# Optimization experiments

Measured on AMD Instinct MI355X. Metric: run time of the kernel, lower is better.

The kernel has to match this reference:

```python
import jax, jax.numpy as jnp
import numpy as np

TOPK = 5
LAMBDA_ALIGN_K = 16.0
MOM = 0.9          # EMA momentum
DEFAULT_SCORE = 0.5  # EMA bank default (bank starts empty)
EPS = 1e-8
NEG = 1.0e9


def pairwise_cosine(X):
    # torch F.normalize: X / max(||X||, eps)
    n = jnp.linalg.norm(X, axis=-1, keepdims=True)
    Xn = X / jnp.maximum(n, EPS)
    sim = Xn @ Xn.T
    return jnp.clip(sim, -1.0 + EPS, 1.0 - EPS)


def knn_mask(sim, allowed_base, topk=TOPK):
    B = sim.shape[0]
    eye = jnp.eye(B, dtype=sim.dtype)
    allowed = allowed_base * (1.0 - eye)
    masked = sim - NEG * eye
    masked = jnp.where(allowed < 0.5, -NEG, masked)
    masked = jnp.where(masked < 0.0, -NEG, masked)
    cand = (masked > 0).sum(axis=1)
    k = min(topk, max(B - 1, 1))
    keep_row = (cand >= topk).astype(sim.dtype)
    keep = keep_row[:, None] * keep_row[None, :]
    idx = jax.lax.top_k(masked, k)[1]                       # [B, k]
    M = jnp.zeros_like(sim).at[jnp.arange(B)[:, None], idx].set(1.0)
    M = jnp.maximum(M, M.T)
    return M * allowed * keep


def build_intra(sim, same, topk=TOPK):
    M = knn_mask(sim, same, topk)
    A = jnp.maximum(sim * M, 0.0) * same
    return A, M


def pga_loss(feats_sub, labels_sub):
    # feats_sub: [L, b, d]
    L = feats_sub.shape[0]
    same = (labels_sub[:, None] == labels_sub[None, :]).astype(jnp.float32)
    sims = jax.vmap(pairwise_cosine)(feats_sub)             # [L, b, b]
    A, M = jax.vmap(lambda s: build_intra(s, same))(sims)   # [L, b, b] each

    # EMA degree-based scores (no-grad in original; bank starts empty so
    # fetch-after-update == mom*default + (1-mom)*score_cur)
    S_intra = jnp.maximum(sims * same, 0.0)
    deg = jnp.maximum((S_intra > 0).sum(axis=2).astype(jnp.float32), 1.0)
    score_cur = jax.nn.sigmoid(S_intra.sum(axis=2) / deg)   # [L, b]
    ema = jax.lax.stop_gradient(MOM * DEFAULT_SCORE + (1.0 - MOM) * score_cur)

    # layer-pair masked MSE alignment, target detached
    A_deep = A[1:]
    A_tgt = jax.lax.stop_gradient(A[:-1])
    M_eff = jnp.maximum(M[:-1], M[1:])                      # [L-1, b, b]
    W = ema[:-1, :, None] * ema[:-1, None, :]               # [L-1, b, b]
    diff2 = (A_deep - A_tgt) ** 2 * W
    num = (diff2 * M_eff).sum(axis=(1, 2))
    den = jnp.maximum((M_eff * W).sum(axis=(1, 2)), EPS)
    terms = jnp.where(M_eff.sum(axis=(1, 2)) > 0, num / den, 0.0)
    raw = terms.sum() / max(L - 1, 1)
    return LAMBDA_ALIGN_K * raw


def setup_inputs() -> dict:
    key = jax.random.key(0)
    k1, k2 = jax.random.split(key)
    feats_final = jax.random.normal(k1, (8, 2048, 512), dtype=jnp.float32)
    labels = jax.random.randint(k2, (2048,), 0, 128).astype(jnp.int64)
    sample_ids = jnp.arange(2048, dtype=jnp.int64)
    return {"feats_final": feats_final, "labels": labels, "sample_ids": sample_ids}


def reference(feats_final, labels, sample_ids):
    # candidate subset from last layer (no-grad in original)
    X_last = feats_final[-1]
    S_last = pairwise_cosine(X_last)
    same_full = (labels[:, None] == labels[None, :]).astype(jnp.float32)
    _, M_last = build_intra(S_last, same_full)
    cand_mask = (M_last > 0).sum(axis=1) > 0
    idx_sub = jnp.nonzero(cand_mask)[0]  # eager (concrete) subselection
    feats_sub = feats_final[:, idx_sub]  # [L, b, d]
    labels_sub = labels[idx_sub]
    return pga_loss(feats_sub, labels_sub)
```

## Files before the change

### kernel.cpp

```cpp
#include <hip/hip_runtime.h>
#include <cmath>

#define NB   2048
#define ND   512
#define NL   8
#define NLAB 128
#define MAXM 64
#define TOPK_ 5
#define NTH  256
#define MAXSLOT 9
#define GSTRIDE (MAXM*MAXM)

#define SLOT_DECL(s) int off##s = -1; int lds##s = 0; float4 pre##s;
#define SLOT_INIT(s) { int idx = tid + (s)*NTH; if (idx < (m << 5)) { \
    int i = idx >> 5, k4 = idx & 31; \
    off##s = (g_s[i] << 9) + (k4 << 2); \
    lds##s = i * 132 + (k4 << 2); \
    pre##s = *(const float4*)(X + off##s); } }
#define SLOT_STORE(s) if (off##s >= 0) *(float4*)(XtF + lds##s) = pre##s;
#define SLOT_FETCH(s, kcn) if (off##s >= 0) pre##s = *(const float4*)(X + off##s + (kcn));

__global__ __launch_bounds__(NTH) void k_gram(
    const float* __restrict__ feats, const int* __restrict__ labels,
    float* __restrict__ G, int* __restrict__ cnt,
    unsigned long long* __restrict__ insub)
{
    __shared__ int wsum[4];
    __shared__ int g_s[MAXM];
    __shared__ float Xt[MAXM][132];
    __shared__ float rinvp[64];
    __shared__ unsigned long long tops_s[64];
    __shared__ unsigned char keep_s[64];
    float* XtF = &Xt[0][0];
    int c = blockIdx.x, l = blockIdx.y, tid = threadIdx.x;
    int lane = tid & 63, wv = tid >> 6;

    int my[8]; int n = 0; int base_i = tid * 8;
    for (int t = 0; t < 8; ++t) {
        int i = base_i + t;
        if (labels[i] == c) my[n++] = i;
    }
    int scan = n;
    #pragma unroll
    for (int off = 1; off < 64; off <<= 1) {
        int v = __shfl_up(scan, off);
        if (lane >= off) scan += v;
    }
    if (lane == 63) wsum[wv] = scan;
    __syncthreads();
    int w0 = wsum[0], w1 = wsum[1], w2 = wsum[2], w3 = wsum[3];
    int m = w0 + w1 + w2 + w3; if (m > MAXM) m = MAXM;
    int base = (wv > 0 ? w0 : 0) + (wv > 1 ? w1 : 0) + (wv > 2 ? w2 : 0);
    int excl = base + scan - n;
    for (int t = 0; t < n; ++t) {
        int slot = excl + t;
        if (slot < MAXM) g_s[slot] = my[t];
    }
    if (l == 0 && tid == 0) cnt[c] = m;
    __syncthreads();
    if (m == 0) {
        if (l == 7 && tid == 0) insub[c] = 0ull;
        return;
    }

    const float* X = feats + (size_t)l * NB * ND;

    SLOT_DECL(0) SLOT_DECL(1) SLOT_DECL(2) SLOT_DECL(3)
    SLOT_DECL(4) SLOT_DECL(5) SLOT_DECL(6) SLOT_DECL(7)
    SLOT_INIT(0) SLOT_INIT(1) SLOT_INIT(2) SLOT_INIT(3)
    SLOT_INIT(4) SLOT_INIT(5) SLOT_INIT(6) SLOT_INIT(7)

    const int P = m * (m + 1) / 2;
    float acc0[MAXSLOT], acc1[MAXSLOT];
    short is_[MAXSLOT], js_[MAXSLOT];
    int ns = 0;
    for (int p = tid; p < P; p += NTH) {
        int i = (int)((sqrtf(8.0f * (float)p + 1.0f) - 1.0f) * 0.5f);
        while (((i + 1) * (i + 2)) / 2 <= p) ++i;
        while ((i * (i + 1)) / 2 > p) --i;
        is_[ns] = (short)i;
        js_[ns] = (short)(p - (i * (i + 1)) / 2);
        acc0[ns] = 0.0f; acc1[ns] = 0.0f;
        ++ns;
    }

    for (int kc = 0; kc < ND; kc += 128) {
        if (kc) __syncthreads();
        SLOT_STORE(0) SLOT_STORE(1) SLOT_STORE(2) SLOT_STORE(3)
        SLOT_STORE(4) SLOT_STORE(5) SLOT_STORE(6) SLOT_STORE(7)
        __syncthreads();
        if (kc + 128 < ND) {
            int kcn = kc + 128;
            SLOT_FETCH(0, kcn) SLOT_FETCH(1, kcn) SLOT_FETCH(2, kcn) SLOT_FETCH(3, kcn)
            SLOT_FETCH(4, kcn) SLOT_FETCH(5, kcn) SLOT_FETCH(6, kcn) SLOT_FETCH(7, kcn)
        }
        for (int s = 0; s < ns; ++s) {
            int i = is_[s], j = js_[s];
            float a0 = acc0[s], a1 = acc1[s];
            #pragma unroll
            for (int k4 = 0; k4 < 32; ++k4) {
                float4 a = *(const float4*)&Xt[i][k4 << 2];
                float4 b = *(const float4*)&Xt[j][k4 << 2];
                a0 = fmaf(a.x, b.x, a0); a1 = fmaf(a.y, b.y, a1);
                a0 = fmaf(a.z, b.z, a0); a1 = fmaf(a.w, b.w, a1);
            }
            acc0[s] = a0; acc1[s] = a1;
        }
    }
    float* Gc = G + ((size_t)l * NLAB + c) * GSTRIDE;
    for (int s = 0; s < ns; ++s) {
        int i = is_[s], j = js_[s];
        float v = acc0[s] + acc1[s];
        Gc[i * MAXM + j] = v;
        Gc[j * MAXM + i] = v;
    }
    if (l != 7) return;

    float (*Gs)[65] = (float(*)[65])(&Xt[0][0]);
    __syncthreads();
    for (int s = 0; s < ns; ++s) {
        int i = is_[s], j = js_[s];
        float v = acc0[s] + acc1[s];
        Gs[i][j] = v; Gs[j][i] = v;
    }
    if (tid < m) for (int j = m; j < 64; ++j) Gs[tid][j] = -2.0f;
    __syncthreads();
    if (tid < 64) {
        rinvp[tid] = (tid < m) ? 1.0f / fmaxf(sqrtf(Gs[tid][tid]), 1e-8f) : 0.0f;
        keep_s[tid] = 0; tops_s[tid] = 0ull;
    }
    __syncthreads();
    unsigned long long tops = 0ull; bool keep = false;
    if (tid < m) {
        float ri = rinvp[tid];
        float v0=-1.f,v1=-1.f,v2=-1.f,v3=-1.f,v4=-1.f;
        int i0=0,i1=0,i2=0,i3=0,i4=0, cand=0;
        #pragma unroll 8
        for (int j = 0; j < 64; ++j) {
            float raw = Gs[tid][j];
            float v = fminf(fmaxf(raw * ri * rinvp[j], -1.0f), 1.0f);
            if (raw == -2.0f) v = -2.0f;
            if (v > 0.0f && j != tid) {
                ++cand;
                if      (v > v0) { v4=v3;i4=i3; v3=v2;i3=i2; v2=v1;i2=i1; v1=v0;i1=i0; v0=v;i0=j; }
                else if (v > v1) { v4=v3;i4=i3; v3=v2;i3=i2; v2=v1;i2=i1; v1=v;i1=j; }
                else if (v > v2) { v4=v3;i4=i3; v3=v2;i3=i2; v2=v;i2=j; }
                else if (v > v3) { v4=v3;i4=i3; v3=v;i3=j; }
                else if (v > v4) { v4=v;i4=j; }
            }
        }
        keep = (cand >= TOPK_);
        if (keep) tops = (1ull<<i0)|(1ull<<i1)|(1ull<<i2)|(1ull<<i3)|(1ull<<i4);
        keep_s[tid] = keep ? 1 : 0; tops_s[tid] = tops;
    }
    __syncthreads();
    unsigned long long Mrow = 0ull;
    if (tid < m && keep) {
        for (int j = 0; j < 64; ++j) {
            if (j == tid || !keep_s[j]) continue;
            if (((tops >> j) & 1ull) || ((tops_s[j] >> tid) & 1ull)) Mrow |= (1ull << j);
        }
    }
    if (tid < 64) {
        unsigned long long b = __ballot(Mrow != 0ull);
        if (tid == 0) insub[c] = b;
    }
}

__device__ __forceinline__ void load_tile(
    const float* __restrict__ Gc, int m, int tid, float (*Gs)[65], float* rinv)
{
    if (tid < 64) rinv[tid] = (tid < m) ? 1.0f / fmaxf(sqrtf(Gc[tid * MAXM + tid]), 1e-8f) : 0.0f;
    __syncthreads();
    int tot = m << 4;
    for (int idx4 = tid; idx4 < tot; idx4 += NTH) {
        int i = idx4 >> 4, j0 = (idx4 & 15) << 2;
        float4 raw = *(const float4*)(Gc + i * MAXM + j0);
        float ri = rinv[i];
        Gs[i][j0 + 0] = (j0 + 0 < m) ? fminf(fmaxf(raw.x * ri * rinv[j0 + 0], -1.0f), 1.0f) : -2.0f;
        Gs[i][j0 + 1] = (j0 + 1 < m) ? fminf(fmaxf(raw.y * ri * rinv[j0 + 1], -1.0f), 1.0f) : -2.0f;
        Gs[i][j0 + 2] = (j0 + 2 < m) ? fminf(fmaxf(raw.z * ri * rinv[j0 + 2], -1.0f), 1.0f) : -2.0f;
        Gs[i][j0 + 3] = (j0 + 3 < m) ? fminf(fmaxf(raw.w * ri * rinv[j0 + 3], -1.0f), 1.0f) : -2.0f;
    }
    __syncthreads();
}

__global__ __launch_bounds__(NTH) void k_decide(
    const float* __restrict__ G, const int* __restrict__ cnt,
    const unsigned long long* __restrict__ insub,
    unsigned long long* __restrict__ Mbits, float* __restrict__ ema)
{
    __shared__ float Gs[64][65];
    __shared__ float rinv[64];
    __shared__ unsigned long long tops_s[64];
    __shared__ unsigned char keep_s[64];
    int c = blockIdx.x, l = blockIdx.y, tid = threadIdx.x;
    int m = cnt[c]; if (m > MAXM) m = MAXM;
    if (m == 0) return;
    unsigned long long sub = insub[c];

    const float* Gc = G + ((size_t)l * NLAB + c) * GSTRIDE;
    load_tile(Gc, m, tid, Gs, rinv);
    if (tid < 64) { keep_s[tid] = 0; tops_s[tid] = 0ull; }
    __syncthreads();
    unsigned long long tops = 0ull; bool keep = false; bool act = false;
    float emaval = 0.0f;
    if (tid < m) {
        act = (sub >> tid) & 1ull;
        if (act) {
            float v0=-1.f,v1=-1.f,v2=-1.f,v3=-1.f,v4=-1.f;
            int i0=0,i1=0,i2=0,i3=0,i4=0, cand=0, dg=0;
            float rs = 0.0f;
            #pragma unroll 8
            for (int j = 0; j < 64; ++j) {
                float v = Gs[tid][j];
                if (!((sub >> j) & 1ull)) v = -2.0f;
                if (v > 0.0f) {
                    rs += v; ++dg;
                    if (j != tid) {
                        ++cand;
                        if      (v > v0) { v4=v3;i4=i3; v3=v2;i3=i2; v2=v1;i2=i1; v1=v0;i1=i0; v0=v;i0=j; }
                        else if (v > v1) { v4=v3;i4=i3; v3=v2;i3=i2; v2=v1;i2=i1; v1=v;i1=j; }
                        else if (v > v2) { v4=v3;i4=i3; v3=v2;i3=i2; v2=v;i2=j; }
                        else if (v > v3) { v4=v3;i4=i3; v3=v;i3=j; }
                        else if (v > v4) { v4=v;i4=j; }
                    }
                }
            }
            keep = (cand >= TOPK_);
            if (keep) tops = (1ull<<i0)|(1ull<<i1)|(1ull<<i2)|(1ull<<i3)|(1ull<<i4);
            float deg = (float)(dg > 0 ? dg : 1);
            float score = 1.0f / (1.0f + expf(-rs / deg));
            emaval = 0.45f + 0.1f * score;
        }
        keep_s[tid] = keep ? 1 : 0; tops_s[tid] = tops;
    }
    __syncthreads();
    if (tid < m) {
        unsigned long long Mrow = 0ull;
        if (keep) {
            for (int j = 0; j < 64; ++j) {
                if (j == tid || !keep_s[j]) continue;
                if (((tops >> j) & 1ull) || ((tops_s[j] >> tid) & 1ull)) Mrow |= (1ull << j);
            }
        }
        Mbits[((size_t)l * NLAB + c) * MAXM + tid] = Mrow;
        ema[((size_t)l * NLAB + c) * MAXM + tid] = emaval;
    }
}

__global__ __launch_bounds__(NTH) void k_pairs(
    const float* __restrict__ G, const int* __restrict__ cnt,
    const unsigned long long* __restrict__ Mbits, const float* __restrict__ ema,
    float* __restrict__ partial)
{
    __shared__ float r0[64], r1[64];
    __shared__ unsigned long long M0s[64], M1s[64];
    __shared__ float es[64];
    __shared__ float red[12];
    int c = blockIdx.x, p = blockIdx.y, tid = threadIdx.x;
    int m = cnt[c]; if (m > MAXM) m = MAXM;
    const float* G0 = G + ((size_t)p       * NLAB + c) * GSTRIDE;
    const float* G1 = G + ((size_t)(p + 1) * NLAB + c) * GSTRIDE;
    if (tid < m) {
        M0s[tid] = Mbits[((size_t)p * NLAB + c) * MAXM + tid];
        M1s[tid] = Mbits[((size_t)(p + 1) * NLAB + c) * MAXM + tid];
        es[tid]  = ema[((size_t)p * NLAB + c) * MAXM + tid];
        r0[tid]  = 1.0f / fmaxf(sqrtf(G0[tid * MAXM + tid]), 1e-8f);
        r1[tid]  = 1.0f / fmaxf(sqrtf(G1[tid * MAXM + tid]), 1e-8f);
    }
    __syncthreads();
    float fn = 0.0f, fd = 0.0f, fc = 0.0f;
    for (int idx = tid; idx < (m << 6); idx += NTH) {
        int i = idx >> 6, j = idx & 63;
        if (j >= m) continue;
        bool b0 = (M0s[i] >> j) & 1ull;
        bool b1 = (M1s[i] >> j) & 1ull;
        if (b0 | b1) {
            float v0 = b0 ? fminf(fmaxf(G0[idx] * r0[i] * r0[j], -1.0f), 1.0f) : 0.0f;
            float v1 = b1 ? fminf(fmaxf(G1[idx] * r1[i] * r1[j], -1.0f), 1.0f) : 0.0f;
            float w = es[i] * es[j];
            float d = v1 - v0;
            fn = fmaf(d * d, w, fn);
            fd += w;
            fc += 1.0f;
        }
    }
    for (int off = 32; off > 0; off >>= 1) {
        fn += __shfl_down(fn, off);
        fd += __shfl_down(fd, off);
        fc += __shfl_down(fc, off);
    }
    int w = tid >> 6;
    if ((tid & 63) == 0) { red[w * 3] = fn; red[w * 3 + 1] = fd; red[w * 3 + 2] = fc; }
    __syncthreads();
    if (tid == 0) {
        float* dst = partial + ((size_t)p * NLAB + c) * 4;
        dst[0] = red[0] + red[3] + red[6] + red[9];
        dst[1] = red[1] + red[4] + red[7] + red[10];
        dst[2] = red[2] + red[5] + red[8] + red[11];
    }
}

__global__ void k_final(const float* __restrict__ partial, float* __restrict__ out)
{
    int tid = threadIdx.x;
    float total = 0.0f;
    for (int p = 0; p < NL - 1; ++p) {
        float n = 0.0f, d = 0.0f, cc = 0.0f;
        for (int c = tid; c < NLAB; c += 64) {
            const float* src = partial + ((size_t)p * NLAB + c) * 4;
            n += src[0]; d += src[1]; cc += src[2];
        }
        for (int off = 32; off > 0; off >>= 1) {
            n += __shfl_down(n, off);
            d += __shfl_down(d, off);
            cc += __shfl_down(cc, off);
        }
        if (tid == 0 && cc > 0.0f) total += n / fmaxf(d, 1e-8f);
    }
    if (tid == 0) out[0] = 16.0f * total / 7.0f;
}

extern "C" void kernel_launch(void* const* d_in, const int* in_sizes, int n_in,
                              void* d_out, int out_size, void* d_ws, size_t ws_size,
                              hipStream_t stream) {
    const float* feats  = (const float*)d_in[0];
    const int*   labels = (const int*)d_in[1];
    char* w = (char*)d_ws;
    size_t gbytes = (size_t)NL * NLAB * GSTRIDE * 4;
    float*    G       = (float*)(w);
    float*    partial = (float*)(w + gbytes);
    int*      cnt     = (int*)(w + gbytes + 14336);
    unsigned long long* insub = (unsigned long long*)(w + gbytes + 14848);
    unsigned long long* Mbits = (unsigned long long*)(w + gbytes + 16384);
    float*    ema     = (float*)(w + gbytes + 16384 + 524288);
    float*    out     = (float*)d_out;

    k_gram  <<<dim3(NLAB, NL), NTH, 0, stream>>>(feats, labels, G, cnt, insub);
    k_decide<<<dim3(NLAB, NL), NTH, 0, stream>>>(G, cnt, insub, Mbits, ema);
    k_pairs <<<dim3(NLAB, NL - 1), NTH, 0, stream>>>(G, cnt, Mbits, ema, partial);
    k_final <<<1, 64, 0, stream>>>(partial, out);
}
```

Before: 131.8 us.

## Register-block Gram accumulation as 2x2 tiles and swizzle block-to-(class,layer) mapping

The Gram kernel now has each thread compute a 2x2 tile of row pairs instead of a single dot product. Each float4 read from shared memory is reused across two outputs, which halves LDS loads per FMA and leaves more independent accumulators in flight. The launch moves to a 1D grid where the block index is scrambled with an odd multiplier, so classes and layers are spread across CUs instead of running in grid order. The cost is more live registers, and when m is odd a stale padding row gets computed and then discarded.

```diff
diff --git a/kernel.cpp b/kernel.cpp
--- a/kernel.cpp
+++ b/kernel.cpp
@@ -8,7 +8,7 @@
 #define MAXM 64
 #define TOPK_ 5
 #define NTH  256
-#define MAXSLOT 9
+#define NSLOT2 3
 #define GSTRIDE (MAXM*MAXM)
 
 #define SLOT_DECL(s) int off##s = -1; int lds##s = 0; float4 pre##s;
@@ -32,7 +32,9 @@
     __shared__ unsigned long long tops_s[64];
     __shared__ unsigned char keep_s[64];
     float* XtF = &Xt[0][0];
-    int c = blockIdx.x, l = blockIdx.y, tid = threadIdx.x;
+    int bswz = (int)((blockIdx.x * 997u) & 1023u);
+    int c = bswz & 127, l = bswz >> 7;
+    int tid = threadIdx.x;
     int lane = tid & 63, wv = tid >> 6;
 
     int my[8]; int n = 0; int base_i = tid * 8;
@@ -70,19 +72,22 @@
     SLOT_INIT(0) SLOT_INIT(1) SLOT_INIT(2) SLOT_INIT(3)
     SLOT_INIT(4) SLOT_INIT(5) SLOT_INIT(6) SLOT_INIT(7)
 
-    const int P = m * (m + 1) / 2;
-    float acc0[MAXSLOT], acc1[MAXSLOT];
-    short is_[MAXSLOT], js_[MAXSLOT];
+    int m2 = (m + 1) >> 1;
+    const int P2 = m2 * (m2 + 1) / 2;
+    float a0[NSLOT2][4], a1[NSLOT2][4];
+    short i2s[NSLOT2], j2s[NSLOT2];
     int ns = 0;
-    for (int p = tid; p < P; p += NTH) {
+    for (int p = tid; p < P2 && ns < NSLOT2; p += NTH) {
         int i = (int)((sqrtf(8.0f * (float)p + 1.0f) - 1.0f) * 0.5f);
         while (((i + 1) * (i + 2)) / 2 <= p) ++i;
         while ((i * (i + 1)) / 2 > p) --i;
-        is_[ns] = (short)i;
-        js_[ns] = (short)(p - (i * (i + 1)) / 2);
-        acc0[ns] = 0.0f; acc1[ns] = 0.0f;
+        i2s[ns] = (short)i;
+        j2s[ns] = (short)(p - (i * (i + 1)) / 2);
         ++ns;
     }
+    #pragma unroll
+    for (int s = 0; s < NSLOT2; ++s)
+        for (int q = 0; q < 4; ++q) { a0[s][q] = 0.0f; a1[s][q] = 0.0f; }
 
     for (int kc = 0; kc < ND; kc += 128) {
         if (kc) __syncthreads();
@@ -94,34 +99,60 @@
             SLOT_FETCH(0, kcn) SLOT_FETCH(1, kcn) SLOT_FETCH(2, kcn) SLOT_FETCH(3, kcn)
             SLOT_FETCH(4, kcn) SLOT_FETCH(5, kcn) SLOT_FETCH(6, kcn) SLOT_FETCH(7, kcn)
         }
-        for (int s = 0; s < ns; ++s) {
-            int i = is_[s], j = js_[s];
-            float a0 = acc0[s], a1 = acc1[s];
+        #pragma unroll
+        for (int s = 0; s < NSLOT2; ++s) {
+            if (s >= ns) break;
+            int ia = i2s[s] << 1, ja = j2s[s] << 1;
+            int ib = ia + 1, jb = ja + 1;
+            float q00a = a0[s][0], q00b = a1[s][0];
+            float q10a = a0[s][1], q10b = a1[s][1];
+            float q01a = a0[s][2], q01b = a1[s][2];
+            float q11a = a0[s][3], q11b = a1[s][3];
             #pragma unroll
             for (int k4 = 0; k4 < 32; ++k4) {
-                float4 a = *(const float4*)&Xt[i][k4 << 2];
-                float4 b = *(const float4*)&Xt[j][k4 << 2];
-                a0 = fmaf(a.x, b.x, a0); a1 = fmaf(a.y, b.y, a1);
-                a0 = fmaf(a.z, b.z, a0); a1 = fmaf(a.w, b.w, a1);
+                float4 A0 = *(const float4*)&Xt[ia][k4 << 2];
+                float4 B0 = *(const float4*)&Xt[ja][k4 << 2];
+                float4 A1 = *(const float4*)&Xt[ib][k4 << 2];
+                float4 B1 = *(const float4*)&Xt[jb][k4 << 2];
+                q00a = fmaf(A0.x, B0.x, q00a); q00b = fmaf(A0.y, B0.y, q00b);
+                q00a = fmaf(A0.z, B0.z, q00a); q00b = fmaf(A0.w, B0.w, q00b);
+                q10a = fmaf(A1.x, B0.x, q10a); q10b = fmaf(A1.y, B0.y, q10b);
+                q10a = fmaf(A1.z, B0.z, q10a); q10b = fmaf(A1.w, B0.w, q10b);
+                q01a = fmaf(A0.x, B1.x, q01a); q01b = fmaf(A0.y, B1.y, q01b);
+                q01a = fmaf(A0.z, B1.z, q01a); q01b = fmaf(A0.w, B1.w, q01b);
+                q11a = fmaf(A1.x, B1.x, q11a); q11b = fmaf(A1.y, B1.y, q11b);
+                q11a = fmaf(A1.z, B1.z, q11a); q11b = fmaf(A1.w, B1.w, q11b);
             }
-            acc0[s] = a0; acc1[s] = a1;
+            a0[s][0] = q00a; a1[s][0] = q00b; a0[s][1] = q10a; a1[s][1] = q10b;
+            a0[s][2] = q01a; a1[s][2] = q01b; a0[s][3] = q11a; a1[s][3] = q11b;
         }
     }
     float* Gc = G + ((size_t)l * NLAB + c) * GSTRIDE;
-    for (int s = 0; s < ns; ++s) {
-        int i = is_[s], j = js_[s];
-        float v = acc0[s] + acc1[s];
-        Gc[i * MAXM + j] = v;
-        Gc[j * MAXM + i] = v;
+    #pragma unroll
+    for (int s = 0; s < NSLOT2; ++s) {
+        if (s >= ns) break;
+        int ia = i2s[s] << 1, ja = j2s[s] << 1;
+        int ib = ia + 1, jb = ja + 1;
+        float v00 = a0[s][0] + a1[s][0];
+        Gc[ia * MAXM + ja] = v00; Gc[ja * MAXM + ia] = v00;
+        if (ib < m) { float v = a0[s][1] + a1[s][1]; Gc[ib * MAXM + ja] = v; Gc[ja * MAXM + ib] = v; }
+        if (jb < m) { float v = a0[s][2] + a1[s][2]; Gc[ia * MAXM + jb] = v; Gc[jb * MAXM + ia] = v; }
+        if (ib < m && jb < m) { float v = a0[s][3] + a1[s][3]; Gc[ib * MAXM + jb] = v; Gc[jb * MAXM + ib] = v; }
     }
     if (l != 7) return;
 
     float (*Gs)[65] = (float(*)[65])(&Xt[0][0]);
     __syncthreads();
-    for (int s = 0; s < ns; ++s) {
-        int i = is_[s], j = js_[s];
-        float v = acc0[s] + acc1[s];
-        Gs[i][j] = v; Gs[j][i] = v;
+    #pragma unroll
+    for (int s = 0; s < NSLOT2; ++s) {
+        if (s >= ns) break;
+        int ia = i2s[s] << 1, ja = j2s[s] << 1;
+        int ib = ia + 1, jb = ja + 1;
+        float v00 = a0[s][0] + a1[s][0];
+        Gs[ia][ja] = v00; Gs[ja][ia] = v00;
+        if (ib < m) { float v = a0[s][1] + a1[s][1]; Gs[ib][ja] = v; Gs[ja][ib] = v; }
+        if (jb < m) { float v = a0[s][2] + a1[s][2]; Gs[ia][jb] = v; Gs[jb][ia] = v; }
+        if (ib < m && jb < m) { float v = a0[s][3] + a1[s][3]; Gs[ib][jb] = v; Gs[jb][ib] = v; }
     }
     if (tid < m) for (int j = m; j < 64; ++j) Gs[tid][j] = -2.0f;
     __syncthreads();
@@ -337,7 +368,7 @@
     float*    ema     = (float*)(w + gbytes + 16384 + 524288);
     float*    out     = (float*)d_out;
 
-    k_gram  <<<dim3(NLAB, NL), NTH, 0, stream>>>(feats, labels, G, cnt, insub);
+    k_gram  <<<1024, NTH, 0, stream>>>(feats, labels, G, cnt, insub);
     k_decide<<<dim3(NLAB, NL), NTH, 0, stream>>>(G, cnt, insub, Mbits, ema);
     k_pairs <<<dim3(NLAB, NL - 1), NTH, 0, stream>>>(G, cnt, Mbits, ema, partial);
     k_final <<<1, 64, 0, stream>>>(partial, out);
```

Result: slower. 280.8 us (+113.1%).

## Register-block Gram computation into 2x2 tiles and swizzle block order

Applied to the files above, without the earlier changes.

The per-class Gram kernel now gives each thread a 2x2 block of output entries instead of single (i,j) pairs. Each loaded row is reused across two products, which halves LDS traffic per FMA and allows fully unrolled fixed slots in place of dynamic arrays. The launch also becomes a 1D grid with a multiplicative swizzle that spreads class and layer blocks across CUs, aiming to balance load from uneven class sizes. In exchange, register pressure per thread rises, and the tile slot count assumes m is at most 64.

```diff
diff --git a/kernel.cpp b/kernel.cpp
--- a/kernel.cpp
+++ b/kernel.cpp
@@ -8,7 +8,6 @@
 #define MAXM 64
 #define TOPK_ 5
 #define NTH  256
-#define MAXSLOT 9
 #define GSTRIDE (MAXM*MAXM)
 
 #define SLOT_DECL(s) int off##s = -1; int lds##s = 0; float4 pre##s;
@@ -20,6 +19,40 @@
 #define SLOT_STORE(s) if (off##s >= 0) *(float4*)(XtF + lds##s) = pre##s;
 #define SLOT_FETCH(s, kcn) if (off##s >= 0) pre##s = *(const float4*)(X + off##s + (kcn));
 
+#define T_DECL(s) int ia##s = 0, ja##s = 0; bool tv##s = false; \
+    float p00a##s=0.f,p00b##s=0.f,p10a##s=0.f,p10b##s=0.f, \
+          p01a##s=0.f,p01b##s=0.f,p11a##s=0.f,p11b##s=0.f;
+#define T_INIT(s) { int p = tid + (s)*NTH; if (p < P2) { \
+    int i = (int)((sqrtf(8.0f * (float)p + 1.0f) - 1.0f) * 0.5f); \
+    while (((i + 1) * (i + 2)) / 2 <= p) ++i; \
+    while ((i * (i + 1)) / 2 > p) --i; \
+    ia##s = i << 1; ja##s = (p - (i * (i + 1)) / 2) << 1; tv##s = true; } }
+#define T_COMP(s) if (tv##s) { \
+    const float* Ra = &Xt[ia##s][0]; const float* Rb = Ra + 132; \
+    const float* Ca = &Xt[ja##s][0]; const float* Cb = Ca + 132; \
+    _Pragma("unroll") \
+    for (int k4 = 0; k4 < 32; ++k4) { \
+        float4 A0 = *(const float4*)(Ra + (k4 << 2)); \
+        float4 B0 = *(const float4*)(Ca + (k4 << 2)); \
+        float4 A1 = *(const float4*)(Rb + (k4 << 2)); \
+        float4 B1 = *(const float4*)(Cb + (k4 << 2)); \
+        p00a##s = fmaf(A0.x, B0.x, p00a##s); p00b##s = fmaf(A0.y, B0.y, p00b##s); \
+        p00a##s = fmaf(A0.z, B0.z, p00a##s); p00b##s = fmaf(A0.w, B0.w, p00b##s); \
+        p10a##s = fmaf(A1.x, B0.x, p10a##s); p10b##s = fmaf(A1.y, B0.y, p10b##s); \
+        p10a##s = fmaf(A1.z, B0.z, p10a##s); p10b##s = fmaf(A1.w, B0.w, p10b##s); \
+        p01a##s = fmaf(A0.x, B1.x, p01a##s); p01b##s = fmaf(A0.y, B1.y, p01b##s); \
+        p01a##s = fmaf(A0.z, B1.z, p01a##s); p01b##s = fmaf(A0.w, B1.w, p01b##s); \
+        p11a##s = fmaf(A1.x, B1.x, p11a##s); p11b##s = fmaf(A1.y, B1.y, p11b##s); \
+        p11a##s = fmaf(A1.z, B1.z, p11a##s); p11b##s = fmaf(A1.w, B1.w, p11b##s); \
+    } }
+#define T_EMIT(s, DST, SR) if (tv##s) { \
+    int ia = ia##s, ja = ja##s, ib = ia + 1, jb = ja + 1; \
+    float v00 = p00a##s + p00b##s; \
+    DST[ia * SR + ja] = v00; DST[ja * SR + ia] = v00; \
+    if (ib < m) { float v = p10a##s + p10b##s; DST[ib * SR + ja] = v; DST[ja * SR + ib] = v; } \
+    if (jb < m) { float v = p01a##s + p01b##s; DST[ia * SR + jb] = v; DST[jb * SR + ia] = v; } \
+    if (ib < m && jb < m) { float v = p11a##s + p11b##s; DST[ib * SR + jb] = v; DST[jb * SR + ib] = v; } }
+
 __global__ __launch_bounds__(NTH) void k_gram(
     const float* __restrict__ feats, const int* __restrict__ labels,
     float* __restrict__ G, int* __restrict__ cnt,
@@ -32,7 +65,9 @@
     __shared__ unsigned long long tops_s[64];
     __shared__ unsigned char keep_s[64];
     float* XtF = &Xt[0][0];
-    int c = blockIdx.x, l = blockIdx.y, tid = threadIdx.x;
+    int bswz = (int)((blockIdx.x * 997u) & 1023u);
+    int c = bswz & 127, l = bswz >> 7;
+    int tid = threadIdx.x;
     int lane = tid & 63, wv = tid >> 6;
 
     int my[8]; int n = 0; int base_i = tid * 8;
@@ -70,19 +105,10 @@
     SLOT_INIT(0) SLOT_INIT(1) SLOT_INIT(2) SLOT_INIT(3)
     SLOT_INIT(4) SLOT_INIT(5) SLOT_INIT(6) SLOT_INIT(7)
 
-    const int P = m * (m + 1) / 2;
-    float acc0[MAXSLOT], acc1[MAXSLOT];
-    short is_[MAXSLOT], js_[MAXSLOT];
-    int ns = 0;
-    for (int p = tid; p < P; p += NTH) {
-        int i = (int)((sqrtf(8.0f * (float)p + 1.0f) - 1.0f) * 0.5f);
-        while (((i + 1) * (i + 2)) / 2 <= p) ++i;
-        while ((i * (i + 1)) / 2 > p) --i;
-        is_[ns] = (short)i;
-        js_[ns] = (short)(p - (i * (i + 1)) / 2);
-        acc0[ns] = 0.0f; acc1[ns] = 0.0f;
-        ++ns;
-    }
+    int m2 = (m + 1) >> 1;
+    const int P2 = m2 * (m2 + 1) / 2;
+    T_DECL(0) T_DECL(1) T_DECL(2)
+    T_INIT(0) T_INIT(1) T_INIT(2)
 
     for (int kc = 0; kc < ND; kc += 128) {
         if (kc) __syncthreads();
@@ -94,35 +120,16 @@
             SLOT_FETCH(0, kcn) SLOT_FETCH(1, kcn) SLOT_FETCH(2, kcn) SLOT_FETCH(3, kcn)
             SLOT_FETCH(4, kcn) SLOT_FETCH(5, kcn) SLOT_FETCH(6, kcn) SLOT_FETCH(7, kcn)
         }
-        for (int s = 0; s < ns; ++s) {
-            int i = is_[s], j = js_[s];
-            float a0 = acc0[s], a1 = acc1[s];
-            #pragma unroll
-            for (int k4 = 0; k4 < 32; ++k4) {
-                float4 a = *(const float4*)&Xt[i][k4 << 2];
-                float4 b = *(const float4*)&Xt[j][k4 << 2];
-                a0 = fmaf(a.x, b.x, a0); a1 = fmaf(a.y, b.y, a1);
-                a0 = fmaf(a.z, b.z, a0); a1 = fmaf(a.w, b.w, a1);
-            }
-            acc0[s] = a0; acc1[s] = a1;
-        }
+        T_COMP(0) T_COMP(1) T_COMP(2)
     }
     float* Gc = G + ((size_t)l * NLAB + c) * GSTRIDE;
-    for (int s = 0; s < ns; ++s) {
-        int i = is_[s], j = js_[s];
-        float v = acc0[s] + acc1[s];
-        Gc[i * MAXM + j] = v;
-        Gc[j * MAXM + i] = v;
-    }
+    T_EMIT(0, Gc, MAXM) T_EMIT(1, Gc, MAXM) T_EMIT(2, Gc, MAXM)
     if (l != 7) return;
 
-    float (*Gs)[65] = (float(*)[65])(&Xt[0][0]);
-    __syncthreads();
-    for (int s = 0; s < ns; ++s) {
-        int i = is_[s], j = js_[s];
-        float v = acc0[s] + acc1[s];
-        Gs[i][j] = v; Gs[j][i] = v;
-    }
+    float* GsF = &Xt[0][0];
+    float (*Gs)[65] = (float(*)[65])GsF;
+    __syncthreads();
+    T_EMIT(0, GsF, 65) T_EMIT(1, GsF, 65) T_EMIT(2, GsF, 65)
     if (tid < m) for (int j = m; j < 64; ++j) Gs[tid][j] = -2.0f;
     __syncthreads();
     if (tid < 64) {
@@ -337,7 +344,7 @@
     float*    ema     = (float*)(w + gbytes + 16384 + 524288);
     float*    out     = (float*)d_out;
 
-    k_gram  <<<dim3(NLAB, NL), NTH, 0, stream>>>(feats, labels, G, cnt, insub);
+    k_gram  <<<1024, NTH, 0, stream>>>(feats, labels, G, cnt, insub);
     k_decide<<<dim3(NLAB, NL), NTH, 0, stream>>>(G, cnt, insub, Mbits, ema);
     k_pairs <<<dim3(NLAB, NL - 1), NTH, 0, stream>>>(G, cnt, Mbits, ema, partial);
     k_final <<<1, 64, 0, stream>>>(partial, out);
```

Result: slower. 136.0 us (+3.2%).
